# Performance work log

Hardware: AMD Instinct MI355X
Metric: run time of the kernel (lower is better)

## Reference

```python
import jax, jax.numpy as jnp
import numpy as np

TEMPERATURE = 0.5
EPSILON = 1e-9


def _l2_normalize(x, eps=1e-12):
    # matches torch F.normalize(p=2, dim=-1): x / max(||x||, eps)
    n = jnp.linalg.norm(x, axis=-1, keepdims=True)
    return x / jnp.maximum(n, eps)


def setup_inputs() -> dict:
    key = jax.random.key(0)
    k1, k2, k3 = jax.random.split(key, 3)
    N, D, V = 8192, 128, 3
    H_consensus = jax.random.normal(k1, (N, D), dtype=jnp.float32)
    S_similarity = jax.random.uniform(k2, (N, N), dtype=jnp.float32)
    H_views = jax.random.normal(k3, (V, N, D), dtype=jnp.float32)
    return {"H_consensus": H_consensus, "S_similarity": S_similarity, "H_views": H_views}


def reference(H_consensus, S_similarity, H_views):
    N = H_consensus.shape[0]
    V = H_views.shape[0]
    Hc = _l2_normalize(H_consensus)            # [N, D]
    Hv = _l2_normalize(H_views)                # [V, N, D]
    sim = jnp.einsum('nd,vmd->vnm', Hc, Hv)    # [V, N, N]
    positive = jnp.diagonal(sim, axis1=1, axis2=2) / TEMPERATURE  # [V, N]
    weights = 1.0 - S_similarity               # [N, N], broadcast over V
    denom = jnp.sum(weights * jnp.exp(sim / TEMPERATURE), axis=-1)  # [V, N]
    denom = jnp.maximum(denom, EPSILON)
    loss = -(positive - jnp.log(denom))        # [V, N]
    return jnp.sum(loss) / (N * V)
```

## Files before the change

kernel.cpp:

```cpp
#include <hip/hip_runtime.h>
#include <hip/hip_bf16.h>

constexpr int kN = 8192;
constexpr int kD = 128;
constexpr int kV = 3;
constexpr int kNV = kV * kN;
constexpr int kNChunk = 512;
constexpr int kIters = kNChunk / 16;
constexpr int kAccStride = 528;

typedef __attribute__((ext_vector_type(8))) short bf16x8;
typedef __attribute__((ext_vector_type(4))) float floatx4;

__device__ __forceinline__ unsigned pack_bf16(float a, float b) {
    unsigned ua = __float_as_uint(a);
    unsigned ub = __float_as_uint(b);
    ua = (ua + 0x7FFFu + ((ua >> 16) & 1u)) >> 16;
    ub = (ub + 0x7FFFu + ((ub >> 16) & 1u)) >> 16;
    return ua | (ub << 16);
}

__global__ void k_normalize(const float* __restrict__ Hc, const float* __restrict__ Hv,
                            unsigned* __restrict__ HcB, unsigned* __restrict__ HvB) {
    int row  = (blockIdx.x * blockDim.x + threadIdx.x) >> 6;
    int lane = threadIdx.x & 63;
    const float* src;
    unsigned* dst;
    float extra;
    if (row < kN) { src = Hc + (size_t)row * kD; dst = HcB + (size_t)row * (kD / 2); extra = 2.0f; }
    else {
        int r = row - kN;
        src = Hv + (size_t)r * kD; dst = HvB + (size_t)r * (kD / 2); extra = 1.0f;
    }
    float2 x = ((const float2*)src)[lane];
    float ss = x.x * x.x + x.y * x.y;
    ss += __shfl_xor(ss, 1);  ss += __shfl_xor(ss, 2);  ss += __shfl_xor(ss, 4);
    ss += __shfl_xor(ss, 8);  ss += __shfl_xor(ss, 16); ss += __shfl_xor(ss, 32);
    float inv = extra * rsqrtf(fmaxf(ss, 1e-24f));
    dst[lane] = pack_bf16(x.x * inv, x.y * inv);
}

__global__ void k_positive(const unsigned* __restrict__ HcB, const unsigned* __restrict__ HvB,
                           float* __restrict__ pos_partial) {
    int row  = (blockIdx.x * blockDim.x + threadIdx.x) >> 6;
    int lane = threadIdx.x & 63;
    int w    = threadIdx.x >> 6;
    int n    = row & (kN - 1);
    unsigned a = HcB[(size_t)n * (kD / 2) + lane];
    unsigned b = HvB[(size_t)row * (kD / 2) + lane];
    float dot = __uint_as_float(a << 16) * __uint_as_float(b << 16)
              + __uint_as_float(a & 0xFFFF0000u) * __uint_as_float(b & 0xFFFF0000u);
    dot += __shfl_xor(dot, 1);  dot += __shfl_xor(dot, 2);  dot += __shfl_xor(dot, 4);
    dot += __shfl_xor(dot, 8);  dot += __shfl_xor(dot, 16); dot += __shfl_xor(dot, 32);
    __shared__ float acc4[4];
    if (lane == 0) acc4[w] = dot;
    __syncthreads();
    if (threadIdx.x == 0)
        atomicAdd(&pos_partial[blockIdx.x & 255], acc4[0] + acc4[1] + acc4[2] + acc4[3]);
}

__launch_bounds__(256, 3)
__global__ void k_main(const unsigned* __restrict__ HcB, const unsigned* __restrict__ HvB,
                       const float* __restrict__ S, float* __restrict__ denom) {
    __shared__ float accum[kV * kAccStride];

    const int tid  = threadIdx.x;
    const int w    = tid >> 6;
    const int lane = tid & 63;
    const int col  = lane & 15;
    const int quad = lane >> 4;
    const int m0w  = blockIdx.x * 64 + w * 16;
    const int nbase = blockIdx.y * kNChunk;

    for (int i = tid; i < kV * kAccStride; i += 256) accum[i] = 0.f;

    bf16x8 afrag[kV][4];
#pragma unroll
    for (int v = 0; v < kV; ++v) {
        const short* rowp = (const short*)HvB + ((size_t)(v * kN + m0w + col)) * kD;
#pragma unroll
        for (int kk = 0; kk < 4; ++kk)
            afrag[v][kk] = *(const bf16x8*)(rowp + kk * 32 + quad * 8);
    }
    __syncthreads();

    const short* hc = (const short*)HcB;

    bf16x8 bCur[4];
#pragma unroll
    for (int kk = 0; kk < 4; ++kk)
        bCur[kk] = *(const bf16x8*)(hc + (size_t)(nbase + col) * kD + kk * 32 + quad * 8);
    float4 sCur = *(const float4*)(S + (size_t)(nbase + col) * kN + m0w + quad * 4);

    for (int it = 0; it < kIters; ++it) {
        int itn = (it + 1 < kIters) ? (it + 1) : 0;
        int n0n = nbase + itn * 16;
        bf16x8 bNxt[4];
#pragma unroll
        for (int kk = 0; kk < 4; ++kk)
            bNxt[kk] = *(const bf16x8*)(hc + (size_t)(n0n + col) * kD + kk * 32 + quad * 8);
        float4 sNxt = *(const float4*)(S + (size_t)(n0n + col) * kN + m0w + quad * 4);

        floatx4 acc0 = {0.f,0.f,0.f,0.f}, acc1 = {0.f,0.f,0.f,0.f}, acc2 = {0.f,0.f,0.f,0.f};
#pragma unroll
        for (int kk = 0; kk < 4; ++kk) {
            acc0 = __builtin_amdgcn_mfma_f32_16x16x32_bf16(afrag[0][kk], bCur[kk], acc0, 0, 0, 0);
            acc1 = __builtin_amdgcn_mfma_f32_16x16x32_bf16(afrag[1][kk], bCur[kk], acc1, 0, 0, 0);
            acc2 = __builtin_amdgcn_mfma_f32_16x16x32_bf16(afrag[2][kk], bCur[kk], acc2, 0, 0, 0);
        }
        float w0 = 1.f - sCur.x, w1 = 1.f - sCur.y, w2 = 1.f - sCur.z, w3 = 1.f - sCur.w;
        float p0 = w0 * __expf(acc0[0]) + w1 * __expf(acc0[1]) + w2 * __expf(acc0[2]) + w3 * __expf(acc0[3]);
        float p1 = w0 * __expf(acc1[0]) + w1 * __expf(acc1[1]) + w2 * __expf(acc1[2]) + w3 * __expf(acc1[3]);
        float p2 = w0 * __expf(acc2[0]) + w1 * __expf(acc2[1]) + w2 * __expf(acc2[2]) + w3 * __expf(acc2[3]);
        p0 += __shfl_xor(p0, 16); p0 += __shfl_xor(p0, 32);
        p1 += __shfl_xor(p1, 16); p1 += __shfl_xor(p1, 32);
        p2 += __shfl_xor(p2, 16); p2 += __shfl_xor(p2, 32);
        float val = (quad == 0) ? p0 : ((quad == 1) ? p1 : p2);
        if (quad < 3)
            atomicAdd(&accum[quad * kAccStride + it * 16 + col], val);
#pragma unroll
        for (int kk = 0; kk < 4; ++kk) bCur[kk] = bNxt[kk];
        sCur = sNxt;
    }
    __syncthreads();
    for (int i = tid; i < kV * kNChunk; i += 256) {
        int v = i / kNChunk, c = i - v * kNChunk;
        atomicAdd(&denom[(size_t)v * kN + nbase + c], accum[v * kAccStride + c]);
    }
}

__global__ void k_final(const float* __restrict__ denom, const float* __restrict__ pos_partial,
                        float* __restrict__ out) {
    int idx  = blockIdx.x * 256 + threadIdx.x;
    int lane = threadIdx.x & 63;
    int w    = threadIdx.x >> 6;
    float val = logf(fmaxf(denom[idx], 1e-9f));
    if (blockIdx.x == 0) val -= pos_partial[threadIdx.x];
    val += __shfl_xor(val, 1);  val += __shfl_xor(val, 2);  val += __shfl_xor(val, 4);
    val += __shfl_xor(val, 8);  val += __shfl_xor(val, 16); val += __shfl_xor(val, 32);
    __shared__ float acc4[4];
    if (lane == 0) acc4[w] = val;
    __syncthreads();
    if (threadIdx.x == 0)
        atomicAdd(out, (acc4[0] + acc4[1] + acc4[2] + acc4[3]) * (1.0f / kNV));
}

extern "C" void kernel_launch(void* const* d_in, const int* in_sizes, int n_in,
                              void* d_out, int out_size, void* d_ws, size_t ws_size,
                              hipStream_t stream) {
    const float* Hc = (const float*)d_in[0];
    const float* S  = (const float*)d_in[1];
    const float* Hv = (const float*)d_in[2];

    unsigned* HcB  = (unsigned*)d_ws;
    unsigned* HvB  = HcB + (size_t)kN * (kD / 2);
    float*    den  = (float*)(HvB + (size_t)kV * kN * (kD / 2));
    float*    posp = den + kNV;
    float*    outF = (float*)d_out;

    hipMemsetAsync(den, 0, ((size_t)kNV + 256) * sizeof(float), stream);
    hipMemsetAsync(outF, 0, sizeof(float), stream);

    k_normalize<<<dim3((kN + kV * kN) / 4), 256, 0, stream>>>(Hc, Hv, HcB, HvB);
    k_positive<<<dim3(kNV / 4), 256, 0, stream>>>(HcB, HvB, posp);
    k_main<<<dim3(kN / 64, kN / kNChunk), dim3(256), 0, stream>>>(HcB, HvB, S, den);
    k_final<<<dim3(kNV / 256), dim3(256), 0, stream>>>(den, posp, outF);
}
```

Measured before the change: 466.0 us.

## Stage S and Hc tiles through double-buffered LDS with coalesced block loads

Instead of each wave loading its own Hc fragments and narrow S slices from global memory, the block cooperatively loads 32-row tiles of S and Hc into double-buffered shared memory with wide contiguous reads, then each wave reads its fragments from LDS. This removes redundant Hc loads across waves and makes S reads coalesced across full 256-byte rows. It adds a block barrier per iteration and more shared memory, which may limit occupancy.

```diff
diff --git a/kernel.cpp b/kernel.cpp
--- a/kernel.cpp
+++ b/kernel.cpp
@@ -6,8 +6,9 @@
 constexpr int kV = 3;
 constexpr int kNV = kV * kN;
 constexpr int kNChunk = 512;
-constexpr int kIters = kNChunk / 16;
-constexpr int kAccStride = 528;
+constexpr int kNTile = 32;
+constexpr int kIters = kNChunk / kNTile;
+constexpr int kAccStride = 529;
 
 typedef __attribute__((ext_vector_type(8))) short bf16x8;
 typedef __attribute__((ext_vector_type(4))) float floatx4;
@@ -62,6 +63,8 @@
 __launch_bounds__(256, 3)
 __global__ void k_main(const unsigned* __restrict__ HcB, const unsigned* __restrict__ HvB,
                        const float* __restrict__ S, float* __restrict__ denom) {
+    __shared__ float Stile[2][kNTile * 68];
+    __shared__ short Htile[2][kNTile * 136];
     __shared__ float accum[kV * kAccStride];
 
     const int tid  = threadIdx.x;
@@ -69,8 +72,11 @@
     const int lane = tid & 63;
     const int col  = lane & 15;
     const int quad = lane >> 4;
-    const int m0w  = blockIdx.x * 64 + w * 16;
+    const int m0b  = blockIdx.x * 64;
+    const int m0w  = m0b + w * 16;
     const int nbase = blockIdx.y * kNChunk;
+    const int sr = tid >> 4;
+    const int sc = tid & 15;
 
     for (int i = tid; i < kV * kAccStride; i += 256) accum[i] = 0.f;
 
@@ -82,49 +88,69 @@
         for (int kk = 0; kk < 4; ++kk)
             afrag[v][kk] = *(const bf16x8*)(rowp + kk * 32 + quad * 8);
     }
-    __syncthreads();
 
     const short* hc = (const short*)HcB;
 
-    bf16x8 bCur[4];
-#pragma unroll
-    for (int kk = 0; kk < 4; ++kk)
-        bCur[kk] = *(const bf16x8*)(hc + (size_t)(nbase + col) * kD + kk * 32 + quad * 8);
-    float4 sCur = *(const float4*)(S + (size_t)(nbase + col) * kN + m0w + quad * 4);
+    {
+        int n0 = nbase;
+        float4 sa = *(const float4*)(S + (size_t)(n0 + sr) * kN + m0b + sc * 4);
+        float4 sb = *(const float4*)(S + (size_t)(n0 + sr + 16) * kN + m0b + sc * 4);
+        float4 ha = *(const float4*)(hc + (size_t)(n0 + sr) * kD + sc * 8);
+        float4 hb = *(const float4*)(hc + (size_t)(n0 + sr + 16) * kD + sc * 8);
+        *(float4*)&Stile[0][sr * 68 + sc * 4]        = sa;
+        *(float4*)&Stile[0][(sr + 16) * 68 + sc * 4] = sb;
+        *(float4*)&Htile[0][sr * 136 + sc * 8]        = ha;
+        *(float4*)&Htile[0][(sr + 16) * 136 + sc * 8] = hb;
+    }
+    __syncthreads();
 
     for (int it = 0; it < kIters; ++it) {
-        int itn = (it + 1 < kIters) ? (it + 1) : 0;
-        int n0n = nbase + itn * 16;
-        bf16x8 bNxt[4];
+        int itn = (it + 1 < kIters) ? it + 1 : it;
+        int n0n = nbase + itn * kNTile;
+        float4 sa = *(const float4*)(S + (size_t)(n0n + sr) * kN + m0b + sc * 4);
+        float4 sb = *(const float4*)(S + (size_t)(n0n + sr + 16) * kN + m0b + sc * 4);
+        float4 ha = *(const float4*)(hc + (size_t)(n0n + sr) * kD + sc * 8);
+        float4 hb = *(const float4*)(hc + (size_t)(n0n + sr + 16) * kD + sc * 8);
+
+        const int cur = it & 1;
 #pragma unroll
-        for (int kk = 0; kk < 4; ++kk)
-            bNxt[kk] = *(const bf16x8*)(hc + (size_t)(n0n + col) * kD + kk * 32 + quad * 8);
-        float4 sNxt = *(const float4*)(S + (size_t)(n0n + col) * kN + m0w + quad * 4);
+        for (int sub = 0; sub < 2; ++sub) {
+            const int nrow = sub * 16 + col;
+            bf16x8 bfrag[4];
+#pragma unroll
+            for (int kk = 0; kk < 4; ++kk)
+                bfrag[kk] = *(const bf16x8*)&Htile[cur][nrow * 136 + kk * 32 + quad * 8];
+            float4 s4 = *(const float4*)&Stile[cur][nrow * 68 + w * 16 + quad * 4];
 
-        floatx4 acc0 = {0.f,0.f,0.f,0.f}, acc1 = {0.f,0.f,0.f,0.f}, acc2 = {0.f,0.f,0.f,0.f};
+            floatx4 acc0 = {0.f,0.f,0.f,0.f}, acc1 = {0.f,0.f,0.f,0.f}, acc2 = {0.f,0.f,0.f,0.f};
 #pragma unroll
-        for (int kk = 0; kk < 4; ++kk) {
-            acc0 = __builtin_amdgcn_mfma_f32_16x16x32_bf16(afrag[0][kk], bCur[kk], acc0, 0, 0, 0);
-            acc1 = __builtin_amdgcn_mfma_f32_16x16x32_bf16(afrag[1][kk], bCur[kk], acc1, 0, 0, 0);
-            acc2 = __builtin_amdgcn_mfma_f32_16x16x32_bf16(afrag[2][kk], bCur[kk], acc2, 0, 0, 0);
+            for (int kk = 0; kk < 4; ++kk) {
+                acc0 = __builtin_amdgcn_mfma_f32_16x16x32_bf16(afrag[0][kk], bfrag[kk], acc0, 0, 0, 0);
+                acc1 = __builtin_amdgcn_mfma_f32_16x16x32_bf16(afrag[1][kk], bfrag[kk], acc1, 0, 0, 0);
+                acc2 = __builtin_amdgcn_mfma_f32_16x16x32_bf16(afrag[2][kk], bfrag[kk], acc2, 0, 0, 0);
+            }
+            float w0 = 1.f - s4.x, w1 = 1.f - s4.y, w2 = 1.f - s4.z, w3 = 1.f - s4.w;
+            float p0 = w0 * __expf(acc0[0]) + w1 * __expf(acc0[1]) + w2 * __expf(acc0[2]) + w3 * __expf(acc0[3]);
+            float p1 = w0 * __expf(acc1[0]) + w1 * __expf(acc1[1]) + w2 * __expf(acc1[2]) + w3 * __expf(acc1[3]);
+            float p2 = w0 * __expf(acc2[0]) + w1 * __expf(acc2[1]) + w2 * __expf(acc2[2]) + w3 * __expf(acc2[3]);
+            p0 += __shfl_xor(p0, 16); p0 += __shfl_xor(p0, 32);
+            p1 += __shfl_xor(p1, 16); p1 += __shfl_xor(p1, 32);
+            p2 += __shfl_xor(p2, 16); p2 += __shfl_xor(p2, 32);
+            float val = (quad == 0) ? p0 : ((quad == 1) ? p1 : p2);
+            if (quad < 3)
+                atomicAdd(&accum[quad * kAccStride + it * kNTile + sub * 16 + col], val);
         }
-        float w0 = 1.f - sCur.x, w1 = 1.f - sCur.y, w2 = 1.f - sCur.z, w3 = 1.f - sCur.w;
-        float p0 = w0 * __expf(acc0[0]) + w1 * __expf(acc0[1]) + w2 * __expf(acc0[2]) + w3 * __expf(acc0[3]);
-        float p1 = w0 * __expf(acc1[0]) + w1 * __expf(acc1[1]) + w2 * __expf(acc1[2]) + w3 * __expf(acc1[3]);
-        float p2 = w0 * __expf(acc2[0]) + w1 * __expf(acc2[1]) + w2 * __expf(acc2[2]) + w3 * __expf(acc2[3]);
-        p0 += __shfl_xor(p0, 16); p0 += __shfl_xor(p0, 32);
-        p1 += __shfl_xor(p1, 16); p1 += __shfl_xor(p1, 32);
-        p2 += __shfl_xor(p2, 16); p2 += __shfl_xor(p2, 32);
-        float val = (quad == 0) ? p0 : ((quad == 1) ? p1 : p2);
-        if (quad < 3)
-            atomicAdd(&accum[quad * kAccStride + it * 16 + col], val);
-#pragma unroll
-        for (int kk = 0; kk < 4; ++kk) bCur[kk] = bNxt[kk];
-        sCur = sNxt;
+
+        const int nxt = cur ^ 1;
+        *(float4*)&Stile[nxt][sr * 68 + sc * 4]        = sa;
+        *(float4*)&Stile[nxt][(sr + 16) * 68 + sc * 4] = sb;
+        *(float4*)&Htile[nxt][sr * 136 + sc * 8]        = ha;
+        *(float4*)&Htile[nxt][(sr + 16) * 136 + sc * 8] = hb;
+        __syncthreads();
     }
-    __syncthreads();
+
     for (int i = tid; i < kV * kNChunk; i += 256) {
-        int v = i / kNChunk, c = i - v * kNChunk;
+        int v = i >> 9, c = i & (kNChunk - 1);
         atomicAdd(&denom[(size_t)v * kN + nbase + c], accum[v * kAccStride + c]);
     }
 }
```

Measured after the change: 431.5 us. -7.4%, faster.

## Hold Hc fragments in registers and stream Hv tiles through double-buffered LDS

Applied to the files above, without the earlier changes.

Restructures the main kernel so each wave keeps two 16-row Hc fragments in registers and iterates over a large m-chunk. The Hv tiles for all views are staged cooperatively through double-buffered LDS, and S loads are prefetched two iterations ahead. Per-row denominators accumulate in registers and are written once with global atomics, replacing the per-iteration LDS atomics. In exchange it adds a block barrier every iteration and lowers occupancy (launch bounds drop from 3 to 2). Each block also now reads S with 32 rows per wave, which changes the global access pattern.

```diff
diff --git a/kernel.cpp b/kernel.cpp
--- a/kernel.cpp
+++ b/kernel.cpp
@@ -5,9 +5,10 @@
 constexpr int kD = 128;
 constexpr int kV = 3;
 constexpr int kNV = kV * kN;
-constexpr int kNChunk = 512;
-constexpr int kIters = kNChunk / 16;
-constexpr int kAccStride = 528;
+constexpr int kMChunks = 8;
+constexpr int kMc = kN / kMChunks;
+constexpr int kIters = kMc / 16;
+constexpr int kNBlk = 128;
 
 typedef __attribute__((ext_vector_type(8))) short bf16x8;
 typedef __attribute__((ext_vector_type(4))) float floatx4;
@@ -18,6 +19,11 @@
     ua = (ua + 0x7FFFu + ((ua >> 16) & 1u)) >> 16;
     ub = (ub + 0x7FFFu + ((ub >> 16) & 1u)) >> 16;
     return ua | (ub << 16);
+}
+
+__device__ __forceinline__ void block_sync_lds() {
+    __builtin_amdgcn_s_waitcnt(0xC07F);
+    __builtin_amdgcn_s_barrier();
 }
 
 __global__ void k_normalize(const float* __restrict__ Hc, const float* __restrict__ Hv,
@@ -59,74 +65,106 @@
         atomicAdd(&pos_partial[blockIdx.x & 255], acc4[0] + acc4[1] + acc4[2] + acc4[3]);
 }
 
-__launch_bounds__(256, 3)
+__launch_bounds__(256, 2)
 __global__ void k_main(const unsigned* __restrict__ HcB, const unsigned* __restrict__ HvB,
                        const float* __restrict__ S, float* __restrict__ denom) {
-    __shared__ float accum[kV * kAccStride];
+    __shared__ short HvT[2][kV][16 * 136];
 
     const int tid  = threadIdx.x;
     const int w    = tid >> 6;
     const int lane = tid & 63;
     const int col  = lane & 15;
     const int quad = lane >> 4;
-    const int m0w  = blockIdx.x * 64 + w * 16;
-    const int nbase = blockIdx.y * kNChunk;
-
-    for (int i = tid; i < kV * kAccStride; i += 256) accum[i] = 0.f;
-
-    bf16x8 afrag[kV][4];
-#pragma unroll
-    for (int v = 0; v < kV; ++v) {
-        const short* rowp = (const short*)HvB + ((size_t)(v * kN + m0w + col)) * kD;
+    const int n0w  = blockIdx.x * kNBlk + w * 32;
+    const int mBase = blockIdx.y * kMc;
+
+    const short* hc = (const short*)HcB;
+    const short* hv = (const short*)HvB;
+
+    bf16x8 bfrag[2][4];
+#pragma unroll
+    for (int ns = 0; ns < 2; ++ns)
 #pragma unroll
         for (int kk = 0; kk < 4; ++kk)
-            afrag[v][kk] = *(const bf16x8*)(rowp + kk * 32 + quad * 8);
+            bfrag[ns][kk] = *(const bf16x8*)(hc + (size_t)(n0w + ns * 16 + col) * kD + kk * 32 + quad * 8);
+
+    const int smRow = tid >> 4;
+    const int smOff = tid & 15;
+
+    const float* sRow0 = S + (size_t)(n0w + col) * kN + mBase + quad * 4;
+    const float* sRow1 = S + (size_t)(n0w + 16 + col) * kN + mBase + quad * 4;
+
+    float4 sBuf[2][2];
+    sBuf[0][0] = *(const float4*)(sRow0);
+    sBuf[0][1] = *(const float4*)(sRow1);
+    sBuf[1][0] = *(const float4*)(sRow0 + 16);
+    sBuf[1][1] = *(const float4*)(sRow1 + 16);
+
+    {
+        const size_t srcBase = (size_t)(mBase + smRow) * kD + smOff * 8;
+#pragma unroll
+        for (int v = 0; v < kV; ++v) {
+            float4 t = *(const float4*)(hv + (size_t)v * kN * kD + srcBase);
+            *(float4*)&HvT[0][v][smRow * 136 + smOff * 8] = t;
+        }
     }
-    __syncthreads();
-
-    const short* hc = (const short*)HcB;
-
-    bf16x8 bCur[4];
-#pragma unroll
-    for (int kk = 0; kk < 4; ++kk)
-        bCur[kk] = *(const bf16x8*)(hc + (size_t)(nbase + col) * kD + kk * 32 + quad * 8);
-    float4 sCur = *(const float4*)(S + (size_t)(nbase + col) * kN + m0w + quad * 4);
+    block_sync_lds();
+
+    float dv[kV][2] = {{0.f, 0.f}, {0.f, 0.f}, {0.f, 0.f}};
 
     for (int it = 0; it < kIters; ++it) {
-        int itn = (it + 1 < kIters) ? (it + 1) : 0;
-        int n0n = nbase + itn * 16;
-        bf16x8 bNxt[4];
-#pragma unroll
-        for (int kk = 0; kk < 4; ++kk)
-            bNxt[kk] = *(const bf16x8*)(hc + (size_t)(n0n + col) * kD + kk * 32 + quad * 8);
-        float4 sNxt = *(const float4*)(S + (size_t)(n0n + col) * kN + m0w + quad * 4);
-
-        floatx4 acc0 = {0.f,0.f,0.f,0.f}, acc1 = {0.f,0.f,0.f,0.f}, acc2 = {0.f,0.f,0.f,0.f};
-#pragma unroll
-        for (int kk = 0; kk < 4; ++kk) {
-            acc0 = __builtin_amdgcn_mfma_f32_16x16x32_bf16(afrag[0][kk], bCur[kk], acc0, 0, 0, 0);
-            acc1 = __builtin_amdgcn_mfma_f32_16x16x32_bf16(afrag[1][kk], bCur[kk], acc1, 0, 0, 0);
-            acc2 = __builtin_amdgcn_mfma_f32_16x16x32_bf16(afrag[2][kk], bCur[kk], acc2, 0, 0, 0);
-        }
-        float w0 = 1.f - sCur.x, w1 = 1.f - sCur.y, w2 = 1.f - sCur.z, w3 = 1.f - sCur.w;
-        float p0 = w0 * __expf(acc0[0]) + w1 * __expf(acc0[1]) + w2 * __expf(acc0[2]) + w3 * __expf(acc0[3]);
-        float p1 = w0 * __expf(acc1[0]) + w1 * __expf(acc1[1]) + w2 * __expf(acc1[2]) + w3 * __expf(acc1[3]);
-        float p2 = w0 * __expf(acc2[0]) + w1 * __expf(acc2[1]) + w2 * __expf(acc2[2]) + w3 * __expf(acc2[3]);
-        p0 += __shfl_xor(p0, 16); p0 += __shfl_xor(p0, 32);
-        p1 += __shfl_xor(p1, 16); p1 += __shfl_xor(p1, 32);
-        p2 += __shfl_xor(p2, 16); p2 += __shfl_xor(p2, 32);
-        float val = (quad == 0) ? p0 : ((quad == 1) ? p1 : p2);
-        if (quad < 3)
-            atomicAdd(&accum[quad * kAccStride + it * 16 + col], val);
-#pragma unroll
-        for (int kk = 0; kk < 4; ++kk) bCur[kk] = bNxt[kk];
-        sCur = sNxt;
+        const int cur = it & 1, nxt = cur ^ 1;
+
+        const int itH = (it + 1 < kIters) ? it + 1 : it;
+        float4 hvReg[kV];
+        {
+            const size_t srcBase = (size_t)(mBase + itH * 16 + smRow) * kD + smOff * 8;
+#pragma unroll
+            for (int v = 0; v < kV; ++v)
+                hvReg[v] = *(const float4*)(hv + (size_t)v * kN * kD + srcBase);
+        }
+
+        const float4 s0 = sBuf[cur][0], s1 = sBuf[cur][1];
+        const float w00 = 1.f - s0.x, w01 = 1.f - s0.y, w02 = 1.f - s0.z, w03 = 1.f - s0.w;
+        const float w10 = 1.f - s1.x, w11 = 1.f - s1.y, w12 = 1.f - s1.z, w13 = 1.f - s1.w;
+        const int itS = (it + 2 < kIters) ? it + 2 : it;
+        sBuf[cur][0] = *(const float4*)(sRow0 + itS * 16);
+        sBuf[cur][1] = *(const float4*)(sRow1 + itS * 16);
+
+#pragma unroll
+        for (int v = 0; v < kV; ++v) {
+            bf16x8 a[4];
+#pragma unroll
+            for (int kk = 0; kk < 4; ++kk)
+                a[kk] = *(const bf16x8*)&HvT[cur][v][col * 136 + kk * 32 + quad * 8];
+            floatx4 acc0 = {0.f, 0.f, 0.f, 0.f}, acc1 = {0.f, 0.f, 0.f, 0.f};
+#pragma unroll
+            for (int kk = 0; kk < 4; ++kk) {
+                acc0 = __builtin_amdgcn_mfma_f32_16x16x32_bf16(a[kk], bfrag[0][kk], acc0, 0, 0, 0);
+                acc1 = __builtin_amdgcn_mfma_f32_16x16x32_bf16(a[kk], bfrag[1][kk], acc1, 0, 0, 0);
+            }
+            dv[v][0] += w00 * __expf(acc0[0]) + w01 * __expf(acc0[1])
+                      + w02 * __expf(acc0[2]) + w03 * __expf(acc0[3]);
+            dv[v][1] += w10 * __expf(acc1[0]) + w11 * __expf(acc1[1])
+                      + w12 * __expf(acc1[2]) + w13 * __expf(acc1[3]);
+        }
+
+#pragma unroll
+        for (int v = 0; v < kV; ++v)
+            *(float4*)&HvT[nxt][v][smRow * 136 + smOff * 8] = hvReg[v];
+        block_sync_lds();
     }
-    __syncthreads();
-    for (int i = tid; i < kV * kNChunk; i += 256) {
-        int v = i / kNChunk, c = i - v * kNChunk;
-        atomicAdd(&denom[(size_t)v * kN + nbase + c], accum[v * kAccStride + c]);
-    }
+
+#pragma unroll
+    for (int v = 0; v < kV; ++v)
+#pragma unroll
+        for (int ns = 0; ns < 2; ++ns) {
+            float p = dv[v][ns];
+            p += __shfl_xor(p, 16);
+            p += __shfl_xor(p, 32);
+            if (quad == 0)
+                atomicAdd(&denom[(size_t)v * kN + n0w + ns * 16 + col], p);
+        }
 }
 
 __global__ void k_final(const float* __restrict__ denom, const float* __restrict__ pos_partial,
@@ -163,6 +201,6 @@
 
     k_normalize<<<dim3((kN + kV * kN) / 4), 256, 0, stream>>>(Hc, Hv, HcB, HvB);
     k_positive<<<dim3(kNV / 4), 256, 0, stream>>>(HcB, HvB, posp);
-    k_main<<<dim3(kN / 64, kN / kNChunk), dim3(256), 0, stream>>>(HcB, HvB, S, den);
+    k_main<<<dim3(kN / kNBlk, kMChunks), dim3(256), 0, stream>>>(HcB, HvB, S, den);
     k_final<<<dim3(kNV / 256), dim3(256), 0, stream>>>(den, posp, outF);
 }
```

Measured after the change: 480.0 us. 1.03x slower.
